# Optimization experiments

Measured on AMD Instinct MI355X. Metric: run time of the kernel, lower is better.

## Reference

```python
import jax, jax.numpy as jnp
import numpy as np

N_NODES = 100000
N_EDGES = 1600000
N_FEAT = 128
HIDDEN = 128
N_GRAPHS = 64
N_CLASSES = 10
BN_EPS = 1e-5


def setup_inputs() -> dict:
    key = jax.random.key(0)
    ks = jax.random.split(key, 24)
    glorot = lambda k, o, i: jax.random.normal(k, (o, i), jnp.float32) * (1.0 / np.sqrt(i))
    inp = {
        'x': jax.random.normal(ks[0], (N_NODES, N_FEAT), jnp.float32),
        'edge_index': jax.random.randint(ks[1], (2, N_EDGES), 0, N_NODES, jnp.int64),
        'batch': jnp.sort(jax.random.randint(ks[2], (N_NODES,), 0, N_GRAPHS, jnp.int64)),
        # GCNConv(128 -> 128)
        'gcn_w': glorot(ks[3], HIDDEN, N_FEAT),
        'gcn_b': jnp.zeros((HIDDEN,), jnp.float32),
        # SAGEConv layers 1, 2: lin_l (aggregated, with bias) + lin_r (root, no bias)
        'sage1_wl': glorot(ks[4], HIDDEN, HIDDEN),
        'sage1_bl': jnp.zeros((HIDDEN,), jnp.float32),
        'sage1_wr': glorot(ks[5], HIDDEN, HIDDEN),
        'sage2_wl': glorot(ks[6], HIDDEN, HIDDEN),
        'sage2_bl': jnp.zeros((HIDDEN,), jnp.float32),
        'sage2_wr': glorot(ks[7], HIDDEN, HIDDEN),
        # ClassifierBase: 128 -> 200 -> 100 -> 50 -> 10
        'clf_w0': glorot(ks[8], 200, HIDDEN), 'clf_b0': jnp.zeros((200,), jnp.float32),
        'clf_w1': glorot(ks[9], 100, 200), 'clf_b1': jnp.zeros((100,), jnp.float32),
        'clf_w2': glorot(ks[10], 50, 100), 'clf_b2': jnp.zeros((50,), jnp.float32),
        'clf_w3': glorot(ks[11], N_CLASSES, 50), 'clf_b3': jnp.zeros((N_CLASSES,), jnp.float32),
        # BatchNorm1d (eval mode, running_mean=0, running_var=1)
        'bn0_g': jnp.ones((200,), jnp.float32), 'bn0_b': jnp.zeros((200,), jnp.float32),
        'bn1_g': jnp.ones((100,), jnp.float32), 'bn1_b': jnp.zeros((100,), jnp.float32),
        'bn2_g': jnp.ones((50,), jnp.float32), 'bn2_b': jnp.zeros((50,), jnp.float32),
    }
    return inp


def _gcn_conv(x, src, dst, W, b):
    # PyG GCNConv: add self loops, symmetric deg^{-1/2} normalization
    xw = x @ W.T                                                  # [N, H]
    ones = jnp.ones(src.shape[0], xw.dtype)
    deg = jax.ops.segment_sum(ones, dst, num_segments=N_NODES) + 1.0  # self loops
    dinv = jax.lax.rsqrt(deg)
    norm = dinv[src] * dinv[dst]                                  # [E]
    out = jax.ops.segment_sum(xw[src] * norm[:, None], dst, num_segments=N_NODES)
    out = out + xw * (dinv * dinv)[:, None]                       # self-loop term deg^{-1}
    return out + b


def _sage_conv(x, src, dst, Wl, bl, Wr):
    # PyG SAGEConv (mean aggr): lin_l(mean_{j->i} x_j) + lin_r(x_i)
    ones = jnp.ones(src.shape[0], x.dtype)
    cnt = jax.ops.segment_sum(ones, dst, num_segments=N_NODES)
    agg = jax.ops.segment_sum(x[src], dst, num_segments=N_NODES)
    agg = agg / jnp.maximum(cnt, 1.0)[:, None]
    return agg @ Wl.T + bl + x @ Wr.T


def _bn_eval(h, g, b):
    # eval-mode BatchNorm1d with running_mean=0, running_var=1
    return h * (g / np.sqrt(1.0 + BN_EPS)) + b


def reference(x, edge_index, batch, gcn_w, gcn_b,
              sage1_wl, sage1_bl, sage1_wr, sage2_wl, sage2_bl, sage2_wr,
              clf_w0, clf_b0, clf_w1, clf_b1, clf_w2, clf_b2, clf_w3, clf_b3,
              bn0_g, bn0_b, bn1_g, bn1_b, bn2_g, bn2_b):
    src, dst = edge_index[0], edge_index[1]
    h = _gcn_conv(x, src, dst, gcn_w, gcn_b)          # act_func is None -> no activation
    h = _sage_conv(h, src, dst, sage1_wl, sage1_bl, sage1_wr)
    h = _sage_conv(h, src, dst, sage2_wl, sage2_bl, sage2_wr)
    # global mean pool over graphs
    gcnt = jax.ops.segment_sum(jnp.ones(h.shape[0], h.dtype), batch, num_segments=N_GRAPHS)
    g = jax.ops.segment_sum(h, batch, num_segments=N_GRAPHS) / jnp.maximum(gcnt, 1.0)[:, None]
    # ClassifierBase (eval: dropout inactive), tanh activation
    g = jnp.tanh(_bn_eval(g @ clf_w0.T + clf_b0, bn0_g, bn0_b))
    g = jnp.tanh(_bn_eval(g @ clf_w1.T + clf_b1, bn1_g, bn1_b))
    g = jnp.tanh(_bn_eval(g @ clf_w2.T + clf_b2, bn2_g, bn2_b))
    logits = g @ clf_w3.T + clf_b3
    return jax.nn.softmax(logits, axis=1)             # [B, n_classes]
```

## Files before the change

kernel.cpp:

```cpp
#include <hip/hip_runtime.h>

#define N_NODES 100000
#define N_EDGES 1600000
#define NGRAPH 64
#define NBIN 391
#define EPB 2560
#define NBLK 625
#define CAPB 6144
#define CAPP 7168
#define PSPLIT 8
#define SETUPBLK 1600

typedef short s8v __attribute__((ext_vector_type(8)));
typedef float f4v __attribute__((ext_vector_type(4)));
typedef float f2v __attribute__((ext_vector_type(2)));

__device__ __forceinline__ float bflo(unsigned u) { return __uint_as_float(u << 16); }
__device__ __forceinline__ float bfhi(unsigned u) { return __uint_as_float(u & 0xffff0000u); }
__device__ __forceinline__ unsigned short f2bf(float f) {
    unsigned u = __float_as_uint(f);
    u += 0x7fffu + ((u >> 16) & 1u);
    return (unsigned short)(u >> 16);
}
__device__ __forceinline__ float bf2f(unsigned short h) { return __uint_as_float(((unsigned)h) << 16); }
__device__ __forceinline__ unsigned pk(float lo, float hi) {
    return (unsigned)f2bf(lo) | ((unsigned)f2bf(hi) << 16);
}
__device__ __forceinline__ float ldv(const void* p, int i, int f32) {
    return f32 ? ((const float*)p)[i] : bf2f(((const unsigned short*)p)[i]);
}
__device__ __forceinline__ f2v up2(unsigned u) {
    f2v t; t.x = bflo(u); t.y = bfhi(u); return t;
}

__global__ __launch_bounds__(256) void k_setup(const unsigned short* __restrict__ x,
                                               const int* __restrict__ ei,
                                               const int* __restrict__ batch,
                                               int* __restrict__ flags,
                                               int* __restrict__ binCur,
                                               int* __restrict__ gstart,
                                               float* __restrict__ pbuf,
                                               float* __restrict__ wbuf,
                                               unsigned* __restrict__ xcvt,
                                               const void* w0, const void* w1,
                                               const void* w2, const void* w3,
                                               const void* b0, const void* bn0g, const void* bn0b,
                                               const void* b1, const void* bn1g, const void* bn1b,
                                               const void* b2, const void* bn2g, const void* bn2b,
                                               const void* b3) {
    __shared__ int cnt[3];
    int tid = threadIdx.x, bid = blockIdx.x;
    if (tid < 3) cnt[tid] = 0;
    __syncthreads();
    unsigned short h = x[tid * 37];
    int e = (h >> 7) & 0xFF;
    if (e >= 100 && e <= 150) atomicAdd(&cnt[0], 1);
    if (bid == 0) {
        if (ei[2 * (tid * 5000) + 1] == 0) atomicAdd(&cnt[1], 1);
        if (batch[2 * (tid * 193) + 1] == 0) atomicAdd(&cnt[2], 1);
    }
    __syncthreads();
    int f = (cnt[0] == 256) ? 0 : 1;
    int i = bid * 256 + tid;
    if (i < 25600) wbuf[i] = ldv(w0, i, f);
    else if (i < 45600) wbuf[i] = ldv(w1, i - 25600, f);
    else if (i < 50600) wbuf[i] = ldv(w2, i - 45600, f);
    else if (i < 51100) wbuf[i] = ldv(w3, i - 50600, f);
    if (f) {
        for (int id = bid * 256 + tid; id < N_NODES * 64; id += SETUPBLK * 256) {
            float2 u = ((const float2*)x)[id];
            xcvt[id] = pk(u.x, u.y);
        }
    }
    if (bid != 0) return;
    int b64 = (cnt[2] == 256) ? 1 : 0;
    if (tid == 0) {
        flags[0] = f;
        flags[1] = (cnt[1] == 256) ? 1 : 0;
        flags[2] = b64;
    }
    for (int k = tid; k < NBIN; k += 256) binCur[k] = k * CAPB;
    if (tid <= NGRAPH) {
        int g = tid, lo = 0, hi = N_NODES;
        while (lo < hi) {
            int mid = (lo + hi) >> 1;
            int v = b64 ? batch[2 * mid] : batch[mid];
            if (v < g) lo = mid + 1;
            else hi = mid;
        }
        gstart[g] = lo;
    }
    const float invs = rsqrtf(1.0f + 1e-5f);
    if (tid < 200) {
        float a = ldv(bn0g, tid, f) * invs;
        pbuf[tid] = a;
        pbuf[200 + tid] = ldv(b0, tid, f) * a + ldv(bn0b, tid, f);
    }
    if (tid < 100) {
        float a = ldv(bn1g, tid, f) * invs;
        pbuf[400 + tid] = a;
        pbuf[500 + tid] = ldv(b1, tid, f) * a + ldv(bn1b, tid, f);
    }
    if (tid < 50) {
        float a = ldv(bn2g, tid, f) * invs;
        pbuf[600 + tid] = a;
        pbuf[650 + tid] = ldv(b2, tid, f) * a + ldv(bn2b, tid, f);
    }
    if (tid < 10) pbuf[700 + tid] = ldv(b3, tid, f);
}

__global__ __launch_bounds__(256) void k_binfill(const int* __restrict__ ei,
                                                 int* __restrict__ binCur,
                                                 unsigned* __restrict__ staging,
                                                 const int* __restrict__ flags) {
    __shared__ int cnt[NBIN];
    __shared__ int lofs[NBIN];
    __shared__ int curL[NBIN];
    __shared__ int basg[NBIN];
    __shared__ int sA[512], sB[512];
    __shared__ int sbuf[EPB];
    __shared__ int dbuf[EPB];
    __shared__ unsigned ebuf[EPB];
    __shared__ unsigned short bbuf[EPB];
    int tid = threadIdx.x;
    int i64 = flags[1];
    int base = blockIdx.x * EPB;
    for (int i = tid; i < NBIN; i += 256) cnt[i] = 0;
    __syncthreads();
    #pragma unroll
    for (int k = 0; k < EPB / 512; ++k) {
        int e = base + k * 512 + tid * 2;
        int s0, s1, d0, d1;
        if (i64) {
            uint4 vs = *(const uint4*)(ei + 2 * (size_t)e);
            uint4 vd = *(const uint4*)(ei + 2 * (size_t)(N_EDGES + e));
            s0 = (int)vs.x; s1 = (int)vs.z;
            d0 = (int)vd.x; d1 = (int)vd.z;
        } else {
            int2 vs = *(const int2*)(ei + (size_t)e);
            int2 vd = *(const int2*)(ei + (size_t)N_EDGES + e);
            s0 = vs.x; s1 = vs.y;
            d0 = vd.x; d1 = vd.y;
        }
        int l = k * 512 + tid * 2;
        sbuf[l] = s0; sbuf[l + 1] = s1;
        dbuf[l] = d0; dbuf[l + 1] = d1;
        if ((unsigned)d0 < N_NODES) atomicAdd(&cnt[d0 >> 8], 1);
        if ((unsigned)d1 < N_NODES) atomicAdd(&cnt[d1 >> 8], 1);
    }
    __syncthreads();
    for (int k = tid; k < 512; k += 256) sA[k] = (k < NBIN) ? cnt[k] : 0;
    __syncthreads();
    int* src = sA;
    int* dst = sB;
    for (int off = 1; off < 512; off <<= 1) {
        for (int k = tid; k < 512; k += 256)
            dst[k] = src[k] + ((k >= off) ? src[k - off] : 0);
        __syncthreads();
        int* t = src; src = dst; dst = t;
    }
    int totE = src[NBIN - 1];
    for (int i = tid; i < NBIN; i += 256) {
        int excl = src[i] - cnt[i];
        lofs[i] = excl;
        curL[i] = excl;
        basg[i] = cnt[i] ? atomicAdd(&binCur[i], cnt[i]) : 0;
    }
    __syncthreads();
    #pragma unroll
    for (int k = 0; k < EPB / 256; ++k) {
        int l = k * 256 + tid;
        int d = dbuf[l];
        int s = sbuf[l];
        if ((unsigned)d < N_NODES) {
            s = min(max(s, 0), N_NODES - 1);
            int p = atomicAdd(&curL[d >> 8], 1);
            ebuf[p] = ((unsigned)(d & 255) << 20) | (unsigned)s;
            bbuf[p] = (unsigned short)(d >> 8);
        }
    }
    __syncthreads();
    for (int i = tid; i < totE; i += 256) {
        int bb = bbuf[i];
        int p = basg[bb] + (i - lofs[bb]);
        if (p < (bb + 1) * CAPB) staging[p] = ebuf[i];
    }
}

__global__ __launch_bounds__(256) void k_csr(const unsigned* __restrict__ staging,
                                             const int* __restrict__ binCur,
                                             int2* __restrict__ rse,
                                             float* __restrict__ dinv,
                                             int* __restrict__ colidx,
                                             unsigned* __restrict__ padA,
                                             unsigned* __restrict__ padB) {
    __shared__ int deg[256];
    __shared__ int s[256];
    __shared__ int cur[256];
    __shared__ int colbuf[CAPP];
    int b = blockIdx.x, tid = threadIdx.x;
    int n0 = b << 8;
    int nend = min(256, N_NODES - n0);
    int runStart = b * CAPB;
    int outStart = b * CAPP;
    int runLen = min(binCur[b] - runStart, CAPB);
    deg[tid] = 0;
    for (int i = tid; i < CAPP; i += 256) colbuf[i] = N_NODES;
    __syncthreads();
    for (int i = tid; i < runLen; i += 256)
        atomicAdd(&deg[staging[runStart + i] >> 20], 1);
    __syncthreads();
    int myDeg = deg[tid];
    int pdeg = (myDeg + 15) & ~15;
    s[tid] = pdeg;
    __syncthreads();
    for (int off = 1; off < 256; off <<= 1) {
        int x2 = (tid >= off) ? s[tid - off] : 0;
        __syncthreads();
        s[tid] += x2;
        __syncthreads();
    }
    int incl = s[tid];
    int lrs = incl - pdeg;
    if (tid < nend) {
        rse[n0 + tid] = make_int2(outStart + lrs, outStart + lrs + myDeg);
        dinv[n0 + tid] = rsqrtf((float)myDeg + 1.0f);
    }
    cur[tid] = lrs;
    __syncthreads();
    for (int i = tid; i < runLen; i += 256) {
        unsigned e = staging[runStart + i];
        int p = atomicAdd(&cur[e >> 20], 1);
        if (p < CAPP) colbuf[p] = (int)(e & 0xFFFFF);
    }
    __syncthreads();
    int ptot = min(s[255], CAPP);
    for (int i = tid; i < ptot; i += 256) colidx[outStart + i] = colbuf[i];
    if (b == 0) {
        if (tid < 64) {
            padA[(size_t)N_NODES * 64 + tid] = 0u;
            padB[(size_t)N_NODES * 64 + tid] = 0u;
        }
        if (tid == 0) dinv[N_NODES] = 0.f;
    }
}

template <int MODE>
__global__ __launch_bounds__(256) void k_agg(const uint4* __restrict__ xsA,
                                             const uint4* __restrict__ xsB,
                                             const int2* __restrict__ rse,
                                             const float* __restrict__ dinv,
                                             unsigned* __restrict__ out,
                                             const int* __restrict__ col,
                                             const int* __restrict__ flags) {
    int lane = threadIdx.x & 63;
    int node = blockIdx.x * 4 + (threadIdx.x >> 6);
    int glane = lane & 15, grp = lane >> 4;
    const uint4* xs = (MODE == 0) ? (flags[0] ? xsB : xsA) : xsA;
    int2 rr = rse[node];
    int rs = rr.x, deg = rr.y - rr.x;
    int pend = rs + ((deg + 15) & ~15);
    f2v a0 = {0.f, 0.f}, a1 = {0.f, 0.f}, a2 = {0.f, 0.f}, a3 = {0.f, 0.f};
    uint4 selfu = make_uint4(0u, 0u, 0u, 0u);
    float di = 0.f;
    if (MODE == 0) {
        selfu = xs[(unsigned)node * 16u + glane];
        di = dinv[node];
    }

    for (int base = rs; base < pend; base += 16) {
        int4 c = *(const int4*)(col + base + grp * 4);
        float dv0, dv1, dv2, dv3;
        if (MODE == 0) {
            dv0 = dinv[c.x]; dv1 = dinv[c.y]; dv2 = dinv[c.z]; dv3 = dinv[c.w];
            c.x = min(c.x, N_NODES - 1); c.y = min(c.y, N_NODES - 1);
            c.z = min(c.z, N_NODES - 1); c.w = min(c.w, N_NODES - 1);
        }
        uint4 u0 = xs[(unsigned)c.x * 16u + glane];
        uint4 u1 = xs[(unsigned)c.y * 16u + glane];
        uint4 u2 = xs[(unsigned)c.z * 16u + glane];
        uint4 u3 = xs[(unsigned)c.w * 16u + glane];
        if (MODE == 0) {
            a0 += dv0 * up2(u0.x); a1 += dv0 * up2(u0.y); a2 += dv0 * up2(u0.z); a3 += dv0 * up2(u0.w);
            a0 += dv1 * up2(u1.x); a1 += dv1 * up2(u1.y); a2 += dv1 * up2(u1.z); a3 += dv1 * up2(u1.w);
            a0 += dv2 * up2(u2.x); a1 += dv2 * up2(u2.y); a2 += dv2 * up2(u2.z); a3 += dv2 * up2(u2.w);
            a0 += dv3 * up2(u3.x); a1 += dv3 * up2(u3.y); a2 += dv3 * up2(u3.z); a3 += dv3 * up2(u3.w);
        } else {
            a0 += up2(u0.x); a1 += up2(u0.y); a2 += up2(u0.z); a3 += up2(u0.w);
            a0 += up2(u1.x); a1 += up2(u1.y); a2 += up2(u1.z); a3 += up2(u1.w);
            a0 += up2(u2.x); a1 += up2(u2.y); a2 += up2(u2.z); a3 += up2(u2.w);
            a0 += up2(u3.x); a1 += up2(u3.y); a2 += up2(u3.z); a3 += up2(u3.w);
        }
    }
    float r[8] = {a0.x, a0.y, a1.x, a1.y, a2.x, a2.y, a3.x, a3.y};
    #pragma unroll
    for (int i = 0; i < 8; ++i) {
        float v = r[i];
        v += __shfl_xor(v, 16, 64);
        v += __shfl_xor(v, 32, 64);
        r[i] = v;
    }
    if (MODE == 0) {
        float d2 = di * di;
        r[0] = di * r[0] + d2 * bflo(selfu.x); r[1] = di * r[1] + d2 * bfhi(selfu.x);
        r[2] = di * r[2] + d2 * bflo(selfu.y); r[3] = di * r[3] + d2 * bfhi(selfu.y);
        r[4] = di * r[4] + d2 * bflo(selfu.z); r[5] = di * r[5] + d2 * bfhi(selfu.z);
        r[6] = di * r[6] + d2 * bflo(selfu.w); r[7] = di * r[7] + d2 * bfhi(selfu.w);
    } else {
        float s = 1.0f / fmaxf((float)deg, 1.0f);
        #pragma unroll
        for (int i = 0; i < 8; ++i) r[i] *= s;
    }
    if (grp == 0) {
        uint4 o;
        o.x = pk(r[0], r[1]); o.y = pk(r[2], r[3]);
        o.z = pk(r[4], r[5]); o.w = pk(r[6], r[7]);
        *(uint4*)(out + (size_t)node * 64 + glane * 4) = o;
    }
}

template <int DUAL>
__global__ __launch_bounds__(512) void k_gemm(const unsigned short* __restrict__ A0,
                                              const void* __restrict__ W0,
                                              const unsigned short* __restrict__ A1,
                                              const void* __restrict__ W1,
                                              const void* __restrict__ bias,
                                              unsigned short* __restrict__ out,
                                              const int* __restrict__ flags) {
    __shared__ __align__(16) unsigned short Ws[128][136];
    int f32 = flags[0];
    int tid = threadIdx.x;
    int lane = tid & 63;
    int wave = tid >> 6;
    int rowbase = blockIdx.x * 128;
    int lr = lane & 15, q = lane >> 4;
    int m0 = wave * 16;
    int arow = rowbase + m0 + lr;
    if (arow > N_NODES) arow = N_NODES;

    f4v acc[8];
    #pragma unroll
    for (int t = 0; t < 8; ++t) acc[t] = (f4v){0.f, 0.f, 0.f, 0.f};

    #pragma unroll
    for (int p = 0; p < (DUAL ? 2 : 1); ++p) {
        const unsigned short* Ap = p ? A1 : A0;
        const void* Wp = p ? W1 : W0;
        if (p) __syncthreads();
        if (!f32) {
            const unsigned short* Wf = (const unsigned short*)Wp;
            #pragma unroll
            for (int it = 0; it < 4; ++it) {
                int chunk = tid + it * 512;
                int r = chunk >> 4, c8 = (chunk & 15) * 8;
                *(uint4*)&Ws[r][c8] = *(const uint4*)(Wf + r * 128 + c8);
            }
        } else {
            const float* Wf = (const float*)Wp;
            #pragma unroll
            for (int it = 0; it < 8; ++it) {
                int chunk = tid + it * 512;
                int r = chunk >> 5, c4 = (chunk & 31) * 4;
                float4 v = *(const float4*)(Wf + r * 128 + c4);
                *(uint2*)&Ws[r][c4] = make_uint2(pk(v.x, v.y), pk(v.z, v.w));
            }
        }
        const unsigned short* Arp = Ap + (size_t)arow * 128;
        s8v a[4];
        #pragma unroll
        for (int k = 0; k < 4; ++k) a[k] = *(const s8v*)(Arp + k * 32 + q * 8);
        __syncthreads();
        #pragma unroll
        for (int k = 0; k < 4; ++k) {
            #pragma unroll
            for (int t = 0; t < 8; ++t) {
                s8v b = *(const s8v*)&Ws[t * 16 + lr][k * 32 + q * 8];
                acc[t] = __builtin_amdgcn_mfma_f32_16x16x32_bf16(a[k], b, acc[t], 0, 0, 0);
            }
        }
    }
    #pragma unroll
    for (int t = 0; t < 8; ++t) {
        int o = t * 16 + lr;
        float bv = ldv(bias, o, f32);
        #pragma unroll
        for (int j = 0; j < 4; ++j) {
            int m = rowbase + m0 + q * 4 + j;
            if (m < N_NODES) out[(size_t)m * 128 + o] = f2bf(acc[t][j] + bv);
        }
    }
}

__global__ __launch_bounds__(256) void k_pool2(const unsigned* __restrict__ h,
                                               const int* __restrict__ gstart,
                                               float* __restrict__ ppool) {
    __shared__ float part[4][128];
    int g = blockIdx.x / PSPLIT, sl = blockIdx.x % PSPLIT;
    int wave = threadIdx.x >> 6, lane = threadIdx.x & 63;
    int s0 = gstart[g], s1 = gstart[g + 1];
    int n = s1 - s0;
    int chunk = (n + PSPLIT - 1) / PSPLIT;
    int r0 = s0 + sl * chunk;
    int r1 = min(r0 + chunk, s1);
    float a0 = 0.f, a1 = 0.f;
    for (int r = r0 + wave; r < r1; r += 4) {
        unsigned u = h[(size_t)r * 64 + lane];
        a0 += bflo(u);
        a1 += bfhi(u);
    }
    part[wave][2 * lane] = a0;
    part[wave][2 * lane + 1] = a1;
    __syncthreads();
    int t = threadIdx.x;
    if (t < 128) {
        float s = part[0][t] + part[1][t] + part[2][t] + part[3][t];
        ppool[(size_t)blockIdx.x * 128 + t] = s;
    }
}

__global__ __launch_bounds__(256) void k_clf(const float* __restrict__ ppool,
                                             const int* __restrict__ gstart,
                                             const float* __restrict__ wbuf,
                                             const float* __restrict__ pbuf,
                                             void* outv, const int* __restrict__ flags) {
    __shared__ float gin[128];
    __shared__ float ha[200];
    __shared__ float hb[100];
    int b = blockIdx.x, t = threadIdx.x;
    if (t < 128) {
        float s = 0.f;
        #pragma unroll
        for (int k = 0; k < PSPLIT; ++k) s += ppool[(size_t)(b * PSPLIT + k) * 128 + t];
        int cnt = gstart[b + 1] - gstart[b];
        gin[t] = s / fmaxf((float)cnt, 1.0f);
    }
    __syncthreads();
    if (t < 200) {
        const float4* wr = (const float4*)(wbuf + t * 128);
        float s = 0.f;
        #pragma unroll
        for (int k = 0; k < 32; ++k) {
            float4 v = wr[k];
            s += v.x * gin[4 * k] + v.y * gin[4 * k + 1] + v.z * gin[4 * k + 2] + v.w * gin[4 * k + 3];
        }
        ha[t] = tanhf(s * pbuf[t] + pbuf[200 + t]);
    }
    __syncthreads();
    if (t < 100) {
        const float4* wr = (const float4*)(wbuf + 25600 + t * 200);
        float s = 0.f;
        #pragma unroll
        for (int k = 0; k < 50; ++k) {
            float4 v = wr[k];
            s += v.x * ha[4 * k] + v.y * ha[4 * k + 1] + v.z * ha[4 * k + 2] + v.w * ha[4 * k + 3];
        }
        hb[t] = tanhf(s * pbuf[400 + t] + pbuf[500 + t]);
    }
    __syncthreads();
    if (t < 50) {
        const float4* wr = (const float4*)(wbuf + 45600 + t * 100);
        float s = 0.f;
        #pragma unroll
        for (int k = 0; k < 25; ++k) {
            float4 v = wr[k];
            s += v.x * hb[4 * k] + v.y * hb[4 * k + 1] + v.z * hb[4 * k + 2] + v.w * hb[4 * k + 3];
        }
        gin[t] = tanhf(s * pbuf[600 + t] + pbuf[650 + t]);
    }
    __syncthreads();
    if (t == 0) {
        int f = flags[0];
        float lg[10];
        float mx = -1e30f;
        #pragma unroll
        for (int c = 0; c < 10; ++c) {
            const float* wr = wbuf + 50600 + c * 50;
            float s = 0.f;
            for (int k = 0; k < 50; ++k) s += wr[k] * gin[k];
            s += pbuf[700 + c];
            lg[c] = s;
            mx = fmaxf(mx, s);
        }
        float sum = 0.f;
        #pragma unroll
        for (int c = 0; c < 10; ++c) {
            lg[c] = __expf(lg[c] - mx);
            sum += lg[c];
        }
        float inv = 1.0f / sum;
        #pragma unroll
        for (int c = 0; c < 10; ++c) {
            float v = lg[c] * inv;
            if (f) ((float*)outv)[b * 10 + c] = v;
            else ((unsigned short*)outv)[b * 10 + c] = f2bf(v);
        }
    }
}

extern "C" void kernel_launch(void* const* d_in, const int* in_sizes, int n_in,
                              void* d_out, int out_size, void* d_ws, size_t ws_size,
                              hipStream_t stream) {
    const unsigned short* x16 = (const unsigned short*)d_in[0];
    const int* ei = (const int*)d_in[1];
    const int* batch = (const int*)d_in[2];

    char* ws = (char*)d_ws;
    size_t off = 0;
    auto alloc = [&](size_t bytes) {
        size_t r = off;
        off = (off + bytes + 255) & ~(size_t)255;
        return r;
    };
    int* flags = (int*)(ws + alloc(256));
    int2* rse = (int2*)(ws + alloc((size_t)N_NODES * 8));
    int* colidx = (int*)(ws + alloc((size_t)NBIN * CAPP * 4 + 4096));
    float* dinv = (float*)(ws + alloc((size_t)(N_NODES + 1) * 4));
    int* binCur = (int*)(ws + alloc(NBIN * 4));
    int* gstart = (int*)(ws + alloc((NGRAPH + 1) * 4));
    float* pbuf = (float*)(ws + alloc(710 * 4));
    float* ppool = (float*)(ws + alloc((size_t)NGRAPH * PSPLIT * 128 * 4));
    float* wbuf = (float*)(ws + alloc(51100 * 4));
    unsigned short* bufA = (unsigned short*)(ws + alloc((size_t)(N_NODES + 1) * 128 * 2));
    unsigned short* bufB = (unsigned short*)(ws + alloc((size_t)(N_NODES + 1) * 128 * 2));
    unsigned* staging = (unsigned*)bufA;

    k_setup<<<SETUPBLK, 256, 0, stream>>>(x16, ei, batch, flags, binCur, gstart, pbuf, wbuf,
                                          (unsigned*)bufB,
                                          d_in[11], d_in[13], d_in[15], d_in[17],
                                          d_in[12], d_in[19], d_in[20],
                                          d_in[14], d_in[21], d_in[22],
                                          d_in[16], d_in[23], d_in[24], d_in[18]);

    k_binfill<<<NBLK, 256, 0, stream>>>(ei, binCur, staging, flags);
    k_csr<<<NBIN, 256, 0, stream>>>(staging, binCur, rse, dinv, colidx,
                                    (unsigned*)bufA, (unsigned*)bufB);

    k_agg<0><<<N_NODES / 4, 256, 0, stream>>>((const uint4*)x16, (const uint4*)bufB,
                                              rse, dinv, (unsigned*)bufA, colidx, flags);
    k_gemm<0><<<(N_NODES + 127) / 128, 512, 0, stream>>>(bufA, d_in[3], nullptr, nullptr,
                                                         d_in[4], bufA, flags);
    k_agg<1><<<N_NODES / 4, 256, 0, stream>>>((const uint4*)bufA, (const uint4*)bufA,
                                              rse, dinv, (unsigned*)bufB, colidx, flags);
    k_gemm<1><<<(N_NODES + 127) / 128, 512, 0, stream>>>(bufB, d_in[5], bufA, d_in[7],
                                                         d_in[6], bufB, flags);
    k_agg<1><<<N_NODES / 4, 256, 0, stream>>>((const uint4*)bufB, (const uint4*)bufB,
                                              rse, dinv, (unsigned*)bufA, colidx, flags);
    k_gemm<1><<<(N_NODES + 127) / 128, 512, 0, stream>>>(bufA, d_in[8], bufB, d_in[10],
                                                         d_in[9], bufA, flags);
    k_pool2<<<NGRAPH * PSPLIT, 256, 0, stream>>>((const unsigned*)bufA, gstart, ppool);
    k_clf<<<NGRAPH, 256, 0, stream>>>(ppool, gstart, wbuf, pbuf, d_out, flags);
}
```

Measured before the change: 460.5 us.

## Merge setup and bin-fill kernels; process four nodes per wave in aggregation

```diff
diff --git a/kernel.cpp b/kernel.cpp
--- a/kernel.cpp
+++ b/kernel.cpp
@@ -6,10 +6,10 @@
 #define NBIN 391
 #define EPB 2560
 #define NBLK 625
+#define WBLK 200
 #define CAPB 6144
 #define CAPP 7168
 #define PSPLIT 8
-#define SETUPBLK 1600
 
 typedef short s8v __attribute__((ext_vector_type(8)));
 typedef float f4v __attribute__((ext_vector_type(4)));
@@ -33,53 +33,129 @@
     f2v t; t.x = bflo(u); t.y = bfhi(u); return t;
 }
 
-__global__ __launch_bounds__(256) void k_setup(const unsigned short* __restrict__ x,
-                                               const int* __restrict__ ei,
-                                               const int* __restrict__ batch,
-                                               int* __restrict__ flags,
-                                               int* __restrict__ binCur,
-                                               int* __restrict__ gstart,
-                                               float* __restrict__ pbuf,
-                                               float* __restrict__ wbuf,
-                                               unsigned* __restrict__ xcvt,
-                                               const void* w0, const void* w1,
-                                               const void* w2, const void* w3,
-                                               const void* b0, const void* bn0g, const void* bn0b,
-                                               const void* b1, const void* bn1g, const void* bn1b,
-                                               const void* b2, const void* bn2g, const void* bn2b,
-                                               const void* b3) {
-    __shared__ int cnt[3];
+__global__ __launch_bounds__(256) void k_prep(const unsigned short* __restrict__ x,
+                                              const int* __restrict__ ei,
+                                              const int* __restrict__ batch,
+                                              int* __restrict__ flags,
+                                              int* __restrict__ binCur,
+                                              int* __restrict__ gstart,
+                                              float* __restrict__ pbuf,
+                                              float* __restrict__ wbuf,
+                                              unsigned* __restrict__ xcvt,
+                                              unsigned* __restrict__ staging,
+                                              const void* w0, const void* w1,
+                                              const void* w2, const void* w3,
+                                              const void* b0, const void* bn0g, const void* bn0b,
+                                              const void* b1, const void* bn1g, const void* bn1b,
+                                              const void* b2, const void* bn2g, const void* bn2b,
+                                              const void* b3) {
     int tid = threadIdx.x, bid = blockIdx.x;
-    if (tid < 3) cnt[tid] = 0;
-    __syncthreads();
-    unsigned short h = x[tid * 37];
-    int e = (h >> 7) & 0xFF;
-    if (e >= 100 && e <= 150) atomicAdd(&cnt[0], 1);
-    if (bid == 0) {
-        if (ei[2 * (tid * 5000) + 1] == 0) atomicAdd(&cnt[1], 1);
-        if (batch[2 * (tid * 193) + 1] == 0) atomicAdd(&cnt[2], 1);
-    }
-    __syncthreads();
-    int f = (cnt[0] == 256) ? 0 : 1;
-    int i = bid * 256 + tid;
+    if (bid < NBLK) {
+        __shared__ int cnt[NBIN];
+        __shared__ int lofs[NBIN];
+        __shared__ int curL[NBIN];
+        __shared__ int basg[NBIN];
+        __shared__ int sA[512], sB[512];
+        __shared__ int sbuf[EPB];
+        __shared__ int dbuf[EPB];
+        __shared__ unsigned ebuf[EPB];
+        __shared__ unsigned short bbuf[EPB];
+        __shared__ int p64;
+        if (tid == 0) p64 = 0;
+        for (int i = tid; i < NBIN; i += 256) cnt[i] = 0;
+        __syncthreads();
+        if (ei[2 * (tid * 5000) + 1] == 0) atomicAdd(&p64, 1);
+        __syncthreads();
+        int i64 = (p64 == 256);
+        int base = bid * EPB;
+        #pragma unroll
+        for (int k = 0; k < EPB / 512; ++k) {
+            int e = base + k * 512 + tid * 2;
+            int s0, s1, d0, d1;
+            if (i64) {
+                uint4 vs = *(const uint4*)(ei + 2 * (size_t)e);
+                uint4 vd = *(const uint4*)(ei + 2 * (size_t)(N_EDGES + e));
+                s0 = (int)vs.x; s1 = (int)vs.z;
+                d0 = (int)vd.x; d1 = (int)vd.z;
+            } else {
+                int2 vs = *(const int2*)(ei + (size_t)e);
+                int2 vd = *(const int2*)(ei + (size_t)N_EDGES + e);
+                s0 = vs.x; s1 = vs.y;
+                d0 = vd.x; d1 = vd.y;
+            }
+            int l = k * 512 + tid * 2;
+            sbuf[l] = s0; sbuf[l + 1] = s1;
+            dbuf[l] = d0; dbuf[l + 1] = d1;
+            if ((unsigned)d0 < N_NODES) atomicAdd(&cnt[d0 >> 8], 1);
+            if ((unsigned)d1 < N_NODES) atomicAdd(&cnt[d1 >> 8], 1);
+        }
+        __syncthreads();
+        for (int k = tid; k < 512; k += 256) sA[k] = (k < NBIN) ? cnt[k] : 0;
+        __syncthreads();
+        int* src = sA;
+        int* dst = sB;
+        for (int off = 1; off < 512; off <<= 1) {
+            for (int k = tid; k < 512; k += 256)
+                dst[k] = src[k] + ((k >= off) ? src[k - off] : 0);
+            __syncthreads();
+            int* t = src; src = dst; dst = t;
+        }
+        int totE = src[NBIN - 1];
+        for (int i = tid; i < NBIN; i += 256) {
+            int excl = src[i] - cnt[i];
+            lofs[i] = excl;
+            curL[i] = excl;
+            basg[i] = i * CAPB + (cnt[i] ? atomicAdd(&binCur[i], cnt[i]) : 0);
+        }
+        __syncthreads();
+        #pragma unroll
+        for (int k = 0; k < EPB / 256; ++k) {
+            int l = k * 256 + tid;
+            int d = dbuf[l];
+            int s = sbuf[l];
+            if ((unsigned)d < N_NODES) {
+                s = min(max(s, 0), N_NODES - 1);
+                int p = atomicAdd(&curL[d >> 8], 1);
+                ebuf[p] = ((unsigned)(d & 255) << 20) | (unsigned)s;
+                bbuf[p] = (unsigned short)(d >> 8);
+            }
+        }
+        __syncthreads();
+        for (int i = tid; i < totE; i += 256) {
+            int bb = bbuf[i];
+            int p = basg[bb] + (i - lofs[bb]);
+            if (p < (bb + 1) * CAPB) staging[p] = ebuf[i];
+        }
+        return;
+    }
+    int wb = bid - NBLK;
+    __shared__ int c0, c2;
+    if (tid == 0) { c0 = 0; c2 = 0; }
+    __syncthreads();
+    unsigned short hh = x[tid * 37];
+    int e = (hh >> 7) & 0xFF;
+    if (e >= 100 && e <= 150) atomicAdd(&c0, 1);
+    if (wb == 0 && batch[2 * (tid * 193) + 1] == 0) atomicAdd(&c2, 1);
+    __syncthreads();
+    int f = (c0 == 256) ? 0 : 1;
+    int i = wb * 256 + tid;
     if (i < 25600) wbuf[i] = ldv(w0, i, f);
     else if (i < 45600) wbuf[i] = ldv(w1, i - 25600, f);
     else if (i < 50600) wbuf[i] = ldv(w2, i - 45600, f);
     else if (i < 51100) wbuf[i] = ldv(w3, i - 50600, f);
     if (f) {
-        for (int id = bid * 256 + tid; id < N_NODES * 64; id += SETUPBLK * 256) {
+        for (int id = wb * 256 + tid; id < N_NODES * 64; id += WBLK * 256) {
             float2 u = ((const float2*)x)[id];
             xcvt[id] = pk(u.x, u.y);
         }
     }
-    if (bid != 0) return;
-    int b64 = (cnt[2] == 256) ? 1 : 0;
+    if (wb != 0) return;
+    int b64 = (c2 == 256) ? 1 : 0;
     if (tid == 0) {
         flags[0] = f;
-        flags[1] = (cnt[1] == 256) ? 1 : 0;
+        flags[1] = 0;
         flags[2] = b64;
     }
-    for (int k = tid; k < NBIN; k += 256) binCur[k] = k * CAPB;
     if (tid <= NGRAPH) {
         int g = tid, lo = 0, hi = N_NODES;
         while (lo < hi) {
@@ -107,84 +183,6 @@
         pbuf[650 + tid] = ldv(b2, tid, f) * a + ldv(bn2b, tid, f);
     }
     if (tid < 10) pbuf[700 + tid] = ldv(b3, tid, f);
-}
-
-__global__ __launch_bounds__(256) void k_binfill(const int* __restrict__ ei,
-                                                 int* __restrict__ binCur,
-                                                 unsigned* __restrict__ staging,
-                                                 const int* __restrict__ flags) {
-    __shared__ int cnt[NBIN];
-    __shared__ int lofs[NBIN];
-    __shared__ int curL[NBIN];
-    __shared__ int basg[NBIN];
-    __shared__ int sA[512], sB[512];
-    __shared__ int sbuf[EPB];
-    __shared__ int dbuf[EPB];
-    __shared__ unsigned ebuf[EPB];
-    __shared__ unsigned short bbuf[EPB];
-    int tid = threadIdx.x;
-    int i64 = flags[1];
-    int base = blockIdx.x * EPB;
-    for (int i = tid; i < NBIN; i += 256) cnt[i] = 0;
-    __syncthreads();
-    #pragma unroll
-    for (int k = 0; k < EPB / 512; ++k) {
-        int e = base + k * 512 + tid * 2;
-        int s0, s1, d0, d1;
-        if (i64) {
-            uint4 vs = *(const uint4*)(ei + 2 * (size_t)e);
-            uint4 vd = *(const uint4*)(ei + 2 * (size_t)(N_EDGES + e));
-            s0 = (int)vs.x; s1 = (int)vs.z;
-            d0 = (int)vd.x; d1 = (int)vd.z;
-        } else {
-            int2 vs = *(const int2*)(ei + (size_t)e);
-            int2 vd = *(const int2*)(ei + (size_t)N_EDGES + e);
-            s0 = vs.x; s1 = vs.y;
-            d0 = vd.x; d1 = vd.y;
-        }
-        int l = k * 512 + tid * 2;
-        sbuf[l] = s0; sbuf[l + 1] = s1;
-        dbuf[l] = d0; dbuf[l + 1] = d1;
-        if ((unsigned)d0 < N_NODES) atomicAdd(&cnt[d0 >> 8], 1);
-        if ((unsigned)d1 < N_NODES) atomicAdd(&cnt[d1 >> 8], 1);
-    }
-    __syncthreads();
-    for (int k = tid; k < 512; k += 256) sA[k] = (k < NBIN) ? cnt[k] : 0;
-    __syncthreads();
-    int* src = sA;
-    int* dst = sB;
-    for (int off = 1; off < 512; off <<= 1) {
-        for (int k = tid; k < 512; k += 256)
-            dst[k] = src[k] + ((k >= off) ? src[k - off] : 0);
-        __syncthreads();
-        int* t = src; src = dst; dst = t;
-    }
-    int totE = src[NBIN - 1];
-    for (int i = tid; i < NBIN; i += 256) {
-        int excl = src[i] - cnt[i];
-        lofs[i] = excl;
-        curL[i] = excl;
-        basg[i] = cnt[i] ? atomicAdd(&binCur[i], cnt[i]) : 0;
-    }
-    __syncthreads();
-    #pragma unroll
-    for (int k = 0; k < EPB / 256; ++k) {
-        int l = k * 256 + tid;
-        int d = dbuf[l];
-        int s = sbuf[l];
-        if ((unsigned)d < N_NODES) {
-            s = min(max(s, 0), N_NODES - 1);
-            int p = atomicAdd(&curL[d >> 8], 1);
-            ebuf[p] = ((unsigned)(d & 255) << 20) | (unsigned)s;
-            bbuf[p] = (unsigned short)(d >> 8);
-        }
-    }
-    __syncthreads();
-    for (int i = tid; i < totE; i += 256) {
-        int bb = bbuf[i];
-        int p = basg[bb] + (i - lofs[bb]);
-        if (p < (bb + 1) * CAPB) staging[p] = ebuf[i];
-    }
 }
 
 __global__ __launch_bounds__(256) void k_csr(const unsigned* __restrict__ staging,
@@ -203,7 +201,7 @@
     int nend = min(256, N_NODES - n0);
     int runStart = b * CAPB;
     int outStart = b * CAPP;
-    int runLen = min(binCur[b] - runStart, CAPB);
+    int runLen = min(binCur[b], CAPB);
     deg[tid] = 0;
     for (int i = tid; i < CAPP; i += 256) colbuf[i] = N_NODES;
     __syncthreads();
@@ -254,68 +252,109 @@
                                              const int* __restrict__ col,
                                              const int* __restrict__ flags) {
     int lane = threadIdx.x & 63;
-    int node = blockIdx.x * 4 + (threadIdx.x >> 6);
+    int wid = blockIdx.x * 4 + (threadIdx.x >> 6);
     int glane = lane & 15, grp = lane >> 4;
     const uint4* xs = (MODE == 0) ? (flags[0] ? xsB : xsA) : xsA;
-    int2 rr = rse[node];
-    int rs = rr.x, deg = rr.y - rr.x;
-    int pend = rs + ((deg + 15) & ~15);
-    f2v a0 = {0.f, 0.f}, a1 = {0.f, 0.f}, a2 = {0.f, 0.f}, a3 = {0.f, 0.f};
-    uint4 selfu = make_uint4(0u, 0u, 0u, 0u);
-    float di = 0.f;
-    if (MODE == 0) {
-        selfu = xs[(unsigned)node * 16u + glane];
-        di = dinv[node];
-    }
-
-    for (int base = rs; base < pend; base += 16) {
-        int4 c = *(const int4*)(col + base + grp * 4);
-        float dv0, dv1, dv2, dv3;
+    #pragma unroll
+    for (int h = 0; h < 2; ++h) {
+        int nodeA = wid * 4 + h * 2;
+        int nodeB = nodeA + 1;
+        int2 ra = rse[nodeA];
+        int2 rb = rse[nodeB];
+        int degA = ra.y - ra.x, degB = rb.y - rb.x;
+        int pendA = ra.x + ((degA + 15) & ~15);
+        int pendB = rb.x + ((degB + 15) & ~15);
+        int rounds = max(pendA - ra.x, pendB - rb.x) >> 4;
+        int baseA = ra.x + grp * 4, baseB = rb.x + grp * 4;
+        f2v aA0 = {0.f, 0.f}, aA1 = {0.f, 0.f}, aA2 = {0.f, 0.f}, aA3 = {0.f, 0.f};
+        f2v aB0 = {0.f, 0.f}, aB1 = {0.f, 0.f}, aB2 = {0.f, 0.f}, aB3 = {0.f, 0.f};
+        uint4 selfA = make_uint4(0u, 0u, 0u, 0u), selfB = make_uint4(0u, 0u, 0u, 0u);
+        float diA = 0.f, diB = 0.f;
         if (MODE == 0) {
-            dv0 = dinv[c.x]; dv1 = dinv[c.y]; dv2 = dinv[c.z]; dv3 = dinv[c.w];
-            c.x = min(c.x, N_NODES - 1); c.y = min(c.y, N_NODES - 1);
-            c.z = min(c.z, N_NODES - 1); c.w = min(c.w, N_NODES - 1);
-        }
-        uint4 u0 = xs[(unsigned)c.x * 16u + glane];
-        uint4 u1 = xs[(unsigned)c.y * 16u + glane];
-        uint4 u2 = xs[(unsigned)c.z * 16u + glane];
-        uint4 u3 = xs[(unsigned)c.w * 16u + glane];
+            selfA = xs[(size_t)nodeA * 16u + glane]; diA = dinv[nodeA];
+            selfB = xs[(size_t)nodeB * 16u + glane]; diB = dinv[nodeB];
+        }
+        for (int r = 0; r < rounds; ++r) {
+            int4 ca = *(const int4*)(col + baseA);
+            int4 cb = *(const int4*)(col + baseB);
+            if (baseA >= pendA) { ca.x = N_NODES; ca.y = N_NODES; ca.z = N_NODES; ca.w = N_NODES; }
+            if (baseB >= pendB) { cb.x = N_NODES; cb.y = N_NODES; cb.z = N_NODES; cb.w = N_NODES; }
+            baseA += 16; baseB += 16;
+            float d0, d1, d2, d3, e0, e1, e2, e3;
+            if (MODE == 0) {
+                d0 = dinv[ca.x]; d1 = dinv[ca.y]; d2 = dinv[ca.z]; d3 = dinv[ca.w];
+                e0 = dinv[cb.x]; e1 = dinv[cb.y]; e2 = dinv[cb.z]; e3 = dinv[cb.w];
+                ca.x = min(ca.x, N_NODES - 1); ca.y = min(ca.y, N_NODES - 1);
+                ca.z = min(ca.z, N_NODES - 1); ca.w = min(ca.w, N_NODES - 1);
+                cb.x = min(cb.x, N_NODES - 1); cb.y = min(cb.y, N_NODES - 1);
+                cb.z = min(cb.z, N_NODES - 1); cb.w = min(cb.w, N_NODES - 1);
+            }
+            uint4 u0 = xs[(size_t)(unsigned)ca.x * 16u + glane];
+            uint4 u1 = xs[(size_t)(unsigned)ca.y * 16u + glane];
+            uint4 u2 = xs[(size_t)(unsigned)ca.z * 16u + glane];
+            uint4 u3 = xs[(size_t)(unsigned)ca.w * 16u + glane];
+            uint4 v0 = xs[(size_t)(unsigned)cb.x * 16u + glane];
+            uint4 v1 = xs[(size_t)(unsigned)cb.y * 16u + glane];
+            uint4 v2 = xs[(size_t)(unsigned)cb.z * 16u + glane];
+            uint4 v3 = xs[(size_t)(unsigned)cb.w * 16u + glane];
+            if (MODE == 0) {
+                aA0 += d0 * up2(u0.x); aA1 += d0 * up2(u0.y); aA2 += d0 * up2(u0.z); aA3 += d0 * up2(u0.w);
+                aA0 += d1 * up2(u1.x); aA1 += d1 * up2(u1.y); aA2 += d1 * up2(u1.z); aA3 += d1 * up2(u1.w);
+                aA0 += d2 * up2(u2.x); aA1 += d2 * up2(u2.y); aA2 += d2 * up2(u2.z); aA3 += d2 * up2(u2.w);
+                aA0 += d3 * up2(u3.x); aA1 += d3 * up2(u3.y); aA2 += d3 * up2(u3.z); aA3 += d3 * up2(u3.w);
+                aB0 += e0 * up2(v0.x); aB1 += e0 * up2(v0.y); aB2 += e0 * up2(v0.z); aB3 += e0 * up2(v0.w);
+                aB0 += e1 * up2(v1.x); aB1 += e1 * up2(v1.y); aB2 += e1 * up2(v1.z); aB3 += e1 * up2(v1.w);
+                aB0 += e2 * up2(v2.x); aB1 += e2 * up2(v2.y); aB2 += e2 * up2(v2.z); aB3 += e2 * up2(v2.w);
+                aB0 += e3 * up2(v3.x); aB1 += e3 * up2(v3.y); aB2 += e3 * up2(v3.z); aB3 += e3 * up2(v3.w);
+            } else {
+                aA0 += up2(u0.x); aA1 += up2(u0.y); aA2 += up2(u0.z); aA3 += up2(u0.w);
+                aA0 += up2(u1.x); aA1 += up2(u1.y); aA2 += up2(u1.z); aA3 += up2(u1.w);
+                aA0 += up2(u2.x); aA1 += up2(u2.y); aA2 += up2(u2.z); aA3 += up2(u2.w);
+                aA0 += up2(u3.x); aA1 += up2(u3.y); aA2 += up2(u3.z); aA3 += up2(u3.w);
+                aB0 += up2(v0.x); aB1 += up2(v0.y); aB2 += up2(v0.z); aB3 += up2(v0.w);
+                aB0 += up2(v1.x); aB1 += up2(v1.y); aB2 += up2(v1.z); aB3 += up2(v1.w);
+                aB0 += up2(v2.x); aB1 += up2(v2.y); aB2 += up2(v2.z); aB3 += up2(v2.w);
+                aB0 += up2(v3.x); aB1 += up2(v3.y); aB2 += up2(v3.z); aB3 += up2(v3.w);
+            }
+        }
+        float rA[8] = {aA0.x, aA0.y, aA1.x, aA1.y, aA2.x, aA2.y, aA3.x, aA3.y};
+        float rB[8] = {aB0.x, aB0.y, aB1.x, aB1.y, aB2.x, aB2.y, aB3.x, aB3.y};
+        #pragma unroll
+        for (int i = 0; i < 8; ++i) {
+            float v = rA[i];
+            v += __shfl_xor(v, 16, 64);
+            v += __shfl_xor(v, 32, 64);
+            rA[i] = v;
+            float w = rB[i];
+            w += __shfl_xor(w, 16, 64);
+            w += __shfl_xor(w, 32, 64);
+            rB[i] = w;
+        }
         if (MODE == 0) {
-            a0 += dv0 * up2(u0.x); a1 += dv0 * up2(u0.y); a2 += dv0 * up2(u0.z); a3 += dv0 * up2(u0.w);
-            a0 += dv1 * up2(u1.x); a1 += dv1 * up2(u1.y); a2 += dv1 * up2(u1.z); a3 += dv1 * up2(u1.w);
-            a0 += dv2 * up2(u2.x); a1 += dv2 * up2(u2.y); a2 += dv2 * up2(u2.z); a3 += dv2 * up2(u2.w);
-            a0 += dv3 * up2(u3.x); a1 += dv3 * up2(u3.y); a2 += dv3 * up2(u3.z); a3 += dv3 * up2(u3.w);
+            float dA2 = diA * diA, dB2 = diB * diB;
+            rA[0] = diA * rA[0] + dA2 * bflo(selfA.x); rA[1] = diA * rA[1] + dA2 * bfhi(selfA.x);
+            rA[2] = diA * rA[2] + dA2 * bflo(selfA.y); rA[3] = diA * rA[3] + dA2 * bfhi(selfA.y);
+            rA[4] = diA * rA[4] + dA2 * bflo(selfA.z); rA[5] = diA * rA[5] + dA2 * bfhi(selfA.z);
+            rA[6] = diA * rA[6] + dA2 * bflo(selfA.w); rA[7] = diA * rA[7] + dA2 * bfhi(selfA.w);
+            rB[0] = diB * rB[0] + dB2 * bflo(selfB.x); rB[1] = diB * rB[1] + dB2 * bfhi(selfB.x);
+            rB[2] = diB * rB[2] + dB2 * bflo(selfB.y); rB[3] = diB * rB[3] + dB2 * bfhi(selfB.y);
+            rB[4] = diB * rB[4] + dB2 * bflo(selfB.z); rB[5] = diB * rB[5] + dB2 * bfhi(selfB.z);
+            rB[6] = diB * rB[6] + dB2 * bflo(selfB.w); rB[7] = diB * rB[7] + dB2 * bfhi(selfB.w);
         } else {
-            a0 += up2(u0.x); a1 += up2(u0.y); a2 += up2(u0.z); a3 += up2(u0.w);
-            a0 += up2(u1.x); a1 += up2(u1.y); a2 += up2(u1.z); a3 += up2(u1.w);
-            a0 += up2(u2.x); a1 += up2(u2.y); a2 += up2(u2.z); a3 += up2(u2.w);
-            a0 += up2(u3.x); a1 += up2(u3.y); a2 += up2(u3.z); a3 += up2(u3.w);
-        }
-    }
-    float r[8] = {a0.x, a0.y, a1.x, a1.y, a2.x, a2.y, a3.x, a3.y};
-    #pragma unroll
-    for (int i = 0; i < 8; ++i) {
-        float v = r[i];
-        v += __shfl_xor(v, 16, 64);
-        v += __shfl_xor(v, 32, 64);
-        r[i] = v;
-    }
-    if (MODE == 0) {
-        float d2 = di * di;
-        r[0] = di * r[0] + d2 * bflo(selfu.x); r[1] = di * r[1] + d2 * bfhi(selfu.x);
-        r[2] = di * r[2] + d2 * bflo(selfu.y); r[3] = di * r[3] + d2 * bfhi(selfu.y);
-        r[4] = di * r[4] + d2 * bflo(selfu.z); r[5] = di * r[5] + d2 * bfhi(selfu.z);
-        r[6] = di * r[6] + d2 * bflo(selfu.w); r[7] = di * r[7] + d2 * bfhi(selfu.w);
-    } else {
-        float s = 1.0f / fmaxf((float)deg, 1.0f);
-        #pragma unroll
-        for (int i = 0; i < 8; ++i) r[i] *= s;
-    }
-    if (grp == 0) {
-        uint4 o;
-        o.x = pk(r[0], r[1]); o.y = pk(r[2], r[3]);
-        o.z = pk(r[4], r[5]); o.w = pk(r[6], r[7]);
-        *(uint4*)(out + (size_t)node * 64 + glane * 4) = o;
+            float sA = 1.0f / fmaxf((float)degA, 1.0f);
+            float sB = 1.0f / fmaxf((float)degB, 1.0f);
+            #pragma unroll
+            for (int i = 0; i < 8; ++i) { rA[i] *= sA; rB[i] *= sB; }
+        }
+        if (grp == 0) {
+            uint4 o;
+            o.x = pk(rA[0], rA[1]); o.y = pk(rA[2], rA[3]);
+            o.z = pk(rA[4], rA[5]); o.w = pk(rA[6], rA[7]);
+            *(uint4*)(out + (size_t)nodeA * 64 + glane * 4) = o;
+            o.x = pk(rB[0], rB[1]); o.y = pk(rB[2], rB[3]);
+            o.z = pk(rB[4], rB[5]); o.w = pk(rB[6], rB[7]);
+            *(uint4*)(out + (size_t)nodeB * 64 + glane * 4) = o;
+        }
     }
 }
 
@@ -513,7 +552,7 @@
     };
     int* flags = (int*)(ws + alloc(256));
     int2* rse = (int2*)(ws + alloc((size_t)N_NODES * 8));
-    int* colidx = (int*)(ws + alloc((size_t)NBIN * CAPP * 4 + 4096));
+    int* colidx = (int*)(ws + alloc((size_t)NBIN * CAPP * 4 + (size_t)CAPP * 4));
     float* dinv = (float*)(ws + alloc((size_t)(N_NODES + 1) * 4));
     int* binCur = (int*)(ws + alloc(NBIN * 4));
     int* gstart = (int*)(ws + alloc((NGRAPH + 1) * 4));
@@ -524,27 +563,26 @@
     unsigned short* bufB = (unsigned short*)(ws + alloc((size_t)(N_NODES + 1) * 128 * 2));
     unsigned* staging = (unsigned*)bufA;
 
-    k_setup<<<SETUPBLK, 256, 0, stream>>>(x16, ei, batch, flags, binCur, gstart, pbuf, wbuf,
-                                          (unsigned*)bufB,
-                                          d_in[11], d_in[13], d_in[15], d_in[17],
-                                          d_in[12], d_in[19], d_in[20],
-                                          d_in[14], d_in[21], d_in[22],
-                                          d_in[16], d_in[23], d_in[24], d_in[18]);
-
-    k_binfill<<<NBLK, 256, 0, stream>>>(ei, binCur, staging, flags);
+    hipMemsetAsync(binCur, 0, NBIN * 4, stream);
+    k_prep<<<NBLK + WBLK, 256, 0, stream>>>(x16, ei, batch, flags, binCur, gstart, pbuf, wbuf,
+                                            (unsigned*)bufB, staging,
+                                            d_in[11], d_in[13], d_in[15], d_in[17],
+                                            d_in[12], d_in[19], d_in[20],
+                                            d_in[14], d_in[21], d_in[22],
+                                            d_in[16], d_in[23], d_in[24], d_in[18]);
     k_csr<<<NBIN, 256, 0, stream>>>(staging, binCur, rse, dinv, colidx,
                                     (unsigned*)bufA, (unsigned*)bufB);
 
-    k_agg<0><<<N_NODES / 4, 256, 0, stream>>>((const uint4*)x16, (const uint4*)bufB,
-                                              rse, dinv, (unsigned*)bufA, colidx, flags);
+    k_agg<0><<<N_NODES / 16, 256, 0, stream>>>((const uint4*)x16, (const uint4*)bufB,
+                                               rse, dinv, (unsigned*)bufA, colidx, flags);
     k_gemm<0><<<(N_NODES + 127) / 128, 512, 0, stream>>>(bufA, d_in[3], nullptr, nullptr,
                                                          d_in[4], bufA, flags);
-    k_agg<1><<<N_NODES / 4, 256, 0, stream>>>((const uint4*)bufA, (const uint4*)bufA,
-                                              rse, dinv, (unsigned*)bufB, colidx, flags);
+    k_agg<1><<<N_NODES / 16, 256, 0, stream>>>((const uint4*)bufA, (const uint4*)bufA,
+                                               rse, dinv, (unsigned*)bufB, colidx, flags);
     k_gemm<1><<<(N_NODES + 127) / 128, 512, 0, stream>>>(bufB, d_in[5], bufA, d_in[7],
                                                          d_in[6], bufB, flags);
-    k_agg<1><<<N_NODES / 4, 256, 0, stream>>>((const uint4*)bufB, (const uint4*)bufB,
-                                              rse, dinv, (unsigned*)bufA, colidx, flags);
+    k_agg<1><<<N_NODES / 16, 256, 0, stream>>>((const uint4*)bufB, (const uint4*)bufB,
+                                               rse, dinv, (unsigned*)bufA, colidx, flags);
     k_gemm<1><<<(N_NODES + 127) / 128, 512, 0, stream>>>(bufA, d_in[8], bufB, d_in[10],
                                                          d_in[9], bufA, flags);
     k_pool2<<<NGRAPH * PSPLIT, 256, 0, stream>>>((const unsigned*)bufA, gstart, ppool);
```

After: 488.6 us. 1.06x slower.
